# Kernel tuning notes

Measured on AMD Instinct MI355X. Metric: run time of the kernel, lower is better.

The kernel has to match this reference:

```python
import jax, jax.numpy as jnp
import numpy as np

F_NODE = 32   # node feature dim
E_ATTR = 8    # edge attribute dim
H_OUT = 64    # h_theta output dim


def setup_inputs() -> dict:
    key = jax.random.key(0)
    k1, k2, k3 = jax.random.split(key, 3)
    B, N = 1, 1024
    adjacency = jax.random.randint(k1, (B, N, N), 0, 2, dtype=jnp.int32)
    node_features = jax.random.normal(k2, (B, N, F_NODE), dtype=jnp.float32)
    edge_attributes = jax.random.normal(k3, (B, N, N, E_ATTR), dtype=jnp.float32)
    kW = jax.random.fold_in(key, 7)
    W = jax.random.normal(kW, (2 * F_NODE + E_ATTR, H_OUT), dtype=jnp.float32) * (1.0 / np.sqrt(2 * F_NODE + E_ATTR))
    b = jnp.zeros((H_OUT,), dtype=jnp.float32)
    return {"adjacency": adjacency, "node_features": node_features,
            "edge_attributes": edge_attributes, "W": W, "b": b}


def reference(adjacency, node_features, edge_attributes, W, b):
    # EdgeConvE: per edge (v, v') compute h_theta(concat([x_v, x_v' - x_v, e_vv']))
    # then aggregate over neighbors v' selected by the dense adjacency.
    # Split W along the concat axis so we never materialize the [B,N,N,2F+E] concat:
    # concat @ W = x_v @ W_self + (x_v' - x_v) @ W_diff + e @ W_edge
    F = node_features.shape[-1]
    W_self, W_diff, W_edge = W[:F], W[F:2 * F], W[2 * F:]
    self_term = node_features @ (W_self - W_diff)            # [B,N,H]
    nbr_term = node_features @ W_diff                        # [B,N,H]
    edge_term = jnp.einsum('bvwe,eh->bvwh', edge_attributes, W_edge)  # [B,N,N,H]
    msg = jax.nn.relu(self_term[:, :, None, :] + nbr_term[:, None, :, :] + edge_term + b)
    A = adjacency.astype(msg.dtype)                          # [B,N,N] 0/1 mask
    out = jnp.einsum('bvw,bvwh->bvh', A, msg)                # sum-aggregate over neighbors
    return out
```

## Files before the change

kernel.cpp:

```cpp
#include <hip/hip_runtime.h>
#include <hip/hip_bf16.h>

#define N 1024
#define F 32
#define H 64
#define EA 8

typedef __attribute__((ext_vector_type(8))) short bf16x8;
typedef __attribute__((ext_vector_type(16))) float f32x16;

union FragAB { bf16x8 v; unsigned u[4]; };

__device__ __forceinline__ unsigned pk(float a, float b) {
    union { __hip_bfloat162 h; unsigned u; } c;
    c.h = __float22bfloat162_rn(float2{a, b});
    return c.u;
}

__global__ __launch_bounds__(256) void precompute_terms(
    const float* __restrict__ X, const float* __restrict__ W, const float* __restrict__ b,
    float* __restrict__ sv, float* __restrict__ nb, float* __restrict__ out)
{
    const int lane = threadIdx.x & 63;
    const int wid  = threadIdx.x >> 6;
    const int v    = blockIdx.x * 4 + wid;

    float4 xr[8];
    const float4* xp = (const float4*)(X + (size_t)v * F);
#pragma unroll
    for (int i = 0; i < 8; ++i) xr[i] = xp[i];
    const float* xf = (const float*)xr;

    float s = b[lane];
    float n = 0.f;
#pragma unroll
    for (int f = 0; f < F; ++f) {
        float ws = W[f * H + lane];
        float wd = W[(F + f) * H + lane];
        s = fmaf(xf[f], ws - wd, s);
        n = fmaf(xf[f], wd, n);
    }
    const int idx = v * H + lane;
    sv[idx]  = s;
    nb[idx]  = n;
    out[idx] = 0.f;
}

__global__ __launch_bounds__(256, 4) void edge_mfma(
    const int* __restrict__ A, const float* __restrict__ Edge, const float* __restrict__ W,
    const float* __restrict__ sv, const float* __restrict__ nb, float* __restrict__ out)
{
    const int lane = threadIdx.x & 63;
    const int wid  = threadIdx.x >> 6;
    const int lg   = lane >> 5;
    const int ln   = lane & 31;
    const int wq   = blockIdx.x & 7;
    const int vch  = blockIdx.x >> 3;
    const int wbase = wq * 128 + wid * 32;
    const int vbase = vch * 8;

    __shared__ float red[8][64];
    for (int i = threadIdx.x; i < 512; i += 256) ((float*)red)[i] = 0.f;

    FragAB bfr[2];
#pragma unroll
    for (int half = 0; half < 2; ++half) {
        const int n = half * 32 + ln;
#pragma unroll
        for (int q = 0; q < 4; ++q) {
            unsigned we = pk(W[(2 * F + 2 * q) * H + n], W[(2 * F + 2 * q + 1) * H + n]);
            bfr[half].u[q] = (lg == 0) ? we : 0u;
        }
    }

    f32x16 cnb[2];
#pragma unroll
    for (int half = 0; half < 2; ++half)
#pragma unroll
        for (int r = 0; r < 16; ++r) {
            const int row = (r & 3) + 8 * (r >> 2) + 4 * lg;
            cnb[half][r] = nb[(size_t)(wbase + row) * H + half * 32 + ln];
        }

    __syncthreads();

    for (int vi = 0; vi < 8; ++vi) {
        const int v = vbase + vi;

        FragAB afr;
        if (lg == 0) {
            const float4* ep = (const float4*)(Edge + ((size_t)v * N + wbase + ln) * EA);
            const float4 e0 = ep[0];
            const float4 e1 = ep[1];
            afr.u[0] = pk(e0.x, e0.y); afr.u[1] = pk(e0.z, e0.w);
            afr.u[2] = pk(e1.x, e1.y); afr.u[3] = pk(e1.z, e1.w);
        } else {
            const int am = A[(size_t)v * N + wbase + ln];
            afr.u[0] = am ? 0x00003f80u : 0xbf803f80u;
            afr.u[1] = 0u; afr.u[2] = 0u; afr.u[3] = 0u;
        }

        FragAB b0 = bfr[0], b1 = bfr[1];
        if (lg == 1) {
            b0.u[0] = pk(sv[(size_t)v * H + ln],      1e30f);
            b1.u[0] = pk(sv[(size_t)v * H + 32 + ln], 1e30f);
        }

        const f32x16 d0 = __builtin_amdgcn_mfma_f32_32x32x16_bf16(afr.v, b0.v, cnb[0], 0, 0, 0);
        float p0 = 0.f;
#pragma unroll
        for (int r = 0; r < 16; ++r) p0 += fmaxf(d0[r], 0.f);

        const f32x16 d1 = __builtin_amdgcn_mfma_f32_32x32x16_bf16(afr.v, b1.v, cnb[1], 0, 0, 0);
        float p1 = 0.f;
#pragma unroll
        for (int r = 0; r < 16; ++r) p1 += fmaxf(d1[r], 0.f);

        atomicAdd(&red[vi][ln], p0);
        atomicAdd(&red[vi][32 + ln], p1);
    }

    __syncthreads();
    for (int i = threadIdx.x; i < 512; i += 256) {
        const int vi = i >> 6, h = i & 63;
        unsafeAtomicAdd(&out[(size_t)(vbase + vi) * H + h], red[vi][h]);
    }
}

extern "C" void kernel_launch(void* const* d_in, const int* in_sizes, int n_in,
                              void* d_out, int out_size, void* d_ws, size_t ws_size,
                              hipStream_t stream) {
    const int*   A    = (const int*)d_in[0];
    const float* X    = (const float*)d_in[1];
    const float* Edge = (const float*)d_in[2];
    const float* W    = (const float*)d_in[3];
    const float* b    = (const float*)d_in[4];
    float* out = (float*)d_out;

    float* sv = (float*)d_ws;
    float* nb = sv + N * H;

    precompute_terms<<<dim3(256), dim3(256), 0, stream>>>(X, W, b, sv, nb, out);
    edge_mfma<<<dim3(1024), dim3(256), 0, stream>>>(A, Edge, W, sv, nb, out);
}
```

Measured before the change: 104.7 us.

## Prefetch edge/adjacency loads across v-loop and replace LDS atomics with partial buffers

Software-pipelines the per-row loop so the edge attribute and adjacency loads for the next row are issued while the current row's MFMAs run, and all lanes load both values to avoid divergent branches. The shared-memory atomicAdd reduction is replaced by per-wave, per-half partial sums written to a larger LDS buffer and summed after the barrier. The two MFMAs are also issued back to back before their ReLU reductions. This targets load latency and LDS atomic contention, at the cost of more registers, more loads per lane (every lane now fetches edges and the mask), and 16KB of LDS that may limit occupancy.

```diff
diff --git a/kernel.cpp b/kernel.cpp
--- a/kernel.cpp
+++ b/kernel.cpp
@@ -59,8 +59,7 @@
     const int wbase = wq * 128 + wid * 32;
     const int vbase = vch * 8;
 
-    __shared__ float red[8][64];
-    for (int i = threadIdx.x; i < 512; i += 256) ((float*)red)[i] = 0.f;
+    __shared__ float part[4][2][8][64];
 
     FragAB bfr[2];
 #pragma unroll
@@ -82,48 +81,60 @@
             cnb[half][r] = nb[(size_t)(wbase + row) * H + half * 32 + ln];
         }
 
-    __syncthreads();
+    const float4* ep = (const float4*)(Edge + ((size_t)vbase * N + wbase + ln) * EA);
+    const int* ap = A + (size_t)vbase * N + wbase + ln;
 
+    float4 eA = ep[0];
+    float4 eB = ep[1];
+    int    am = ap[0];
+
+#pragma unroll
     for (int vi = 0; vi < 8; ++vi) {
+        const float4 ca = eA;
+        const float4 cb = eB;
+        const int   cam = am;
+        if (vi < 7) {
+            eA = ep[(vi + 1) * 2048];
+            eB = ep[(vi + 1) * 2048 + 1];
+            am = ap[(size_t)(vi + 1) * N];
+        }
         const int v = vbase + vi;
+        const unsigned sp0 = pk(sv[(size_t)v * H + ln],      1e30f);
+        const unsigned sp1 = pk(sv[(size_t)v * H + 32 + ln], 1e30f);
 
         FragAB afr;
-        if (lg == 0) {
-            const float4* ep = (const float4*)(Edge + ((size_t)v * N + wbase + ln) * EA);
-            const float4 e0 = ep[0];
-            const float4 e1 = ep[1];
-            afr.u[0] = pk(e0.x, e0.y); afr.u[1] = pk(e0.z, e0.w);
-            afr.u[2] = pk(e1.x, e1.y); afr.u[3] = pk(e1.z, e1.w);
-        } else {
-            const int am = A[(size_t)v * N + wbase + ln];
-            afr.u[0] = am ? 0x00003f80u : 0xbf803f80u;
-            afr.u[1] = 0u; afr.u[2] = 0u; afr.u[3] = 0u;
-        }
+        const unsigned mpat = cam ? 0x00003f80u : 0xbf803f80u;
+        afr.u[0] = (lg == 0) ? pk(ca.x, ca.y) : mpat;
+        afr.u[1] = (lg == 0) ? pk(ca.z, ca.w) : 0u;
+        afr.u[2] = (lg == 0) ? pk(cb.x, cb.y) : 0u;
+        afr.u[3] = (lg == 0) ? pk(cb.z, cb.w) : 0u;
 
         FragAB b0 = bfr[0], b1 = bfr[1];
-        if (lg == 1) {
-            b0.u[0] = pk(sv[(size_t)v * H + ln],      1e30f);
-            b1.u[0] = pk(sv[(size_t)v * H + 32 + ln], 1e30f);
-        }
+        if (lg) { b0.u[0] = sp0; b1.u[0] = sp1; }
 
         const f32x16 d0 = __builtin_amdgcn_mfma_f32_32x32x16_bf16(afr.v, b0.v, cnb[0], 0, 0, 0);
-        float p0 = 0.f;
+        const f32x16 d1 = __builtin_amdgcn_mfma_f32_32x32x16_bf16(afr.v, b1.v, cnb[1], 0, 0, 0);
+
+        float p0 = 0.f, p1 = 0.f;
 #pragma unroll
-        for (int r = 0; r < 16; ++r) p0 += fmaxf(d0[r], 0.f);
-
-        const f32x16 d1 = __builtin_amdgcn_mfma_f32_32x32x16_bf16(afr.v, b1.v, cnb[1], 0, 0, 0);
-        float p1 = 0.f;
-#pragma unroll
-        for (int r = 0; r < 16; ++r) p1 += fmaxf(d1[r], 0.f);
-
-        atomicAdd(&red[vi][ln], p0);
-        atomicAdd(&red[vi][32 + ln], p1);
+        for (int r = 0; r < 16; ++r) {
+            p0 += fmaxf(d0[r], 0.f);
+            p1 += fmaxf(d1[r], 0.f);
+        }
+        part[wid][lg][vi][ln]      = p0;
+        part[wid][lg][vi][32 + ln] = p1;
     }
 
     __syncthreads();
+#pragma unroll
     for (int i = threadIdx.x; i < 512; i += 256) {
         const int vi = i >> 6, h = i & 63;
-        unsafeAtomicAdd(&out[(size_t)(vbase + vi) * H + h], red[vi][h]);
+        float s = 0.f;
+#pragma unroll
+        for (int w4 = 0; w4 < 4; ++w4)
+#pragma unroll
+            for (int g = 0; g < 2; ++g) s += part[w4][g][vi][h];
+        unsafeAtomicAdd(&out[(size_t)(vbase + vi) * H + h], s);
     }
 }
 
```

New measurement: 89.58 us. -14.4%, faster.
